# Kernel tuning notes

Hardware: AMD Instinct MI355X
Metric: run time of the kernel (lower is better)

The kernel has to match this reference:

```python
import jax, jax.numpy as jnp
import numpy as np

B, T, C = 2, 2048, 1024
N_HEAD, N_KV_HEAD, N_GLOBAL_HEAD = 16, 8, 8
HEAD_DIM = C // N_HEAD  # 64
Q_PER_KV = N_HEAD // N_KV_HEAD  # 2
N_GLOBAL_KV = N_GLOBAL_HEAD // Q_PER_KV  # 4
VE_GATE_CH = 32


def setup_inputs() -> dict:
    key = jax.random.key(0)
    ks = jax.random.split(key, 8)
    x = jax.random.normal(ks[0], (B, T, C), jnp.float32)
    ve = jax.random.normal(ks[1], (B, T, N_KV_HEAD * HEAD_DIM), jnp.float32)
    # rotary cos/sin: [T, 1, head_dim//2]
    half = HEAD_DIM // 2
    inv_freq = 1.0 / (10000.0 ** (np.arange(half, dtype=np.float32) / half))
    ang = np.arange(T, dtype=np.float32)[:, None] * inv_freq[None, :]
    cos = jnp.asarray(np.cos(ang))[:, None, :]
    sin = jnp.asarray(np.sin(ang))[:, None, :]
    s = 0.02
    Wq = jax.random.normal(ks[2], (C, N_HEAD * HEAD_DIM), jnp.float32) * s
    Wk = jax.random.normal(ks[3], (C, N_KV_HEAD * HEAD_DIM), jnp.float32) * s
    Wv = jax.random.normal(ks[4], (C, N_KV_HEAD * HEAD_DIM), jnp.float32) * s
    Wproj = jax.random.normal(ks[5], (C, C), jnp.float32) * s
    Wgate = jax.random.normal(ks[6], (VE_GATE_CH, N_KV_HEAD), jnp.float32) * s
    return {"x": x, "ve": ve, "cos": cos, "sin": sin, "Wq": Wq, "Wk": Wk,
            "Wv": Wv, "Wproj": Wproj, "Wgate": Wgate, "window": 512}


def _rope(x, cos, sin):
    # x: [B,T,H,D]; cos/sin: [T,1,D/2]
    d = x.shape[-1] // 2
    x1, x2 = x[..., :d], x[..., d:]
    return jnp.concatenate([x1 * cos + x2 * sin, -x1 * sin + x2 * cos], axis=-1)


def _rmsnorm(x):
    eps = jnp.finfo(x.dtype).eps
    return x * jax.lax.rsqrt(jnp.mean(x * x, axis=-1, keepdims=True) + eps)


def _attn(q, k, v, mask):
    # q,k,v: [B,T,H,D]; mask: [T,T] bool (True = allowed)
    scale = 1.0 / jnp.sqrt(jnp.asarray(q.shape[-1], q.dtype))
    scores = jnp.einsum('bqhd,bkhd->bhqk', q, k) * scale
    scores = jnp.where(mask[None, None], scores, jnp.finfo(scores.dtype).min)
    p = jax.nn.softmax(scores, axis=-1)
    return jnp.einsum('bhqk,bkhd->bqhd', p, v)


def reference(x, ve, cos, sin, Wq, Wk, Wv, Wproj, Wgate, window):
    q = (x @ Wq).reshape(B, T, N_HEAD, HEAD_DIM)
    k = (x @ Wk).reshape(B, T, N_KV_HEAD, HEAD_DIM)
    v = (x @ Wv).reshape(B, T, N_KV_HEAD, HEAD_DIM)
    # value-embedding gate
    gate = 2.0 * jax.nn.sigmoid(x[..., :VE_GATE_CH] @ Wgate)  # [B,T,n_kv]
    v = v + gate[..., None] * ve.reshape(B, T, N_KV_HEAD, HEAD_DIM)
    q, k = _rope(q, cos, sin), _rope(k, cos, sin)
    q, k = _rmsnorm(q), _rmsnorm(k)
    # split global / local heads
    qg, ql = q[:, :, :N_GLOBAL_HEAD], q[:, :, N_GLOBAL_HEAD:]
    kg, kl = k[:, :, :N_GLOBAL_KV], k[:, :, N_GLOBAL_KV:]
    vg, vl = v[:, :, :N_GLOBAL_KV], v[:, :, N_GLOBAL_KV:]
    # GQA: expand kv heads
    kg, vg = jnp.repeat(kg, Q_PER_KV, axis=2), jnp.repeat(vg, Q_PER_KV, axis=2)
    kl, vl = jnp.repeat(kl, Q_PER_KV, axis=2), jnp.repeat(vl, Q_PER_KV, axis=2)
    i = jnp.arange(T)[:, None]
    j = jnp.arange(T)[None, :]
    causal = j <= i
    local_mask = causal & (j >= i - window)  # flash window_size=(window, 0)
    yg = _attn(qg, kg, vg, causal)
    yl = _attn(ql, kl, vl, local_mask)
    y = jnp.concatenate([yg, yl], axis=2).reshape(B, T, C)
    return y @ Wproj
```

## Files before the change

kernel.cpp:

```cpp
#include <hip/hip_runtime.h>
#include <hip/hip_bf16.h>

#define BB 2
#define TT 2048
#define CC 1024
#define NH 16
#define NKV 8
#define HD 64

typedef __attribute__((ext_vector_type(8))) short short8;
typedef __attribute__((ext_vector_type(4))) float float4v;
typedef __attribute__((ext_vector_type(4))) unsigned int uint4v;

__device__ __forceinline__ ushort f2bf(float f) {
    __hip_bfloat16 h = __float2bfloat16(f);
    union { __hip_bfloat16 h; ushort u; } v; v.h = h; return v.u;
}
__device__ __forceinline__ float bf2f(ushort u) {
    union { unsigned int i; float f; } v; v.i = ((unsigned int)u) << 16; return v.f;
}

__device__ __forceinline__ float fexp2(float x) {
#if __has_builtin(__builtin_amdgcn_exp2f)
    return __builtin_amdgcn_exp2f(x);
#else
    return __expf(x * 0.69314718056f);
#endif
}

__device__ __forceinline__ void gload16(const ushort* g, ushort* l) {
    __builtin_amdgcn_global_load_lds(
        (const __attribute__((address_space(1))) unsigned int*)g,
        (__attribute__((address_space(3))) unsigned int*)l, 16, 0, 0);
}

__device__ __forceinline__ void transpose_tile(
    const float* __restrict__ src, ushort* __restrict__ dst,
    int Kd, int Nd, int kt, int nt, float* tile )
{
    const int tid = threadIdx.x;
    {
        int r = tid >> 2, c = (tid & 3) * 16;
        #pragma unroll
        for (int i = 0; i < 4; i++) {
            float4 v = *(const float4*)&src[(size_t)(kt + r) * Nd + nt + c + i * 4];
            tile[r * 65 + c + i * 4 + 0] = v.x;
            tile[r * 65 + c + i * 4 + 1] = v.y;
            tile[r * 65 + c + i * 4 + 2] = v.z;
            tile[r * 65 + c + i * 4 + 3] = v.w;
        }
    }
    __syncthreads();
    {
        int n = tid >> 2, k = (tid & 3) * 16;
        #pragma unroll
        for (int i = 0; i < 2; i++) {
            ushort u[8];
            #pragma unroll
            for (int j = 0; j < 8; j++) u[j] = f2bf(tile[(k + i * 8 + j) * 65 + n]);
            *(uint4*)&dst[(size_t)(nt + n) * Kd + kt + k + i * 8] = *(uint4*)u;
        }
    }
}

__global__ __launch_bounds__(256) void prep_kernel(
    const float* __restrict__ x, ushort* __restrict__ xb,
    const float* __restrict__ Wq, const float* __restrict__ Wk,
    const float* __restrict__ Wv, const float* __restrict__ Wproj,
    const float* __restrict__ wgate,
    ushort* __restrict__ WqkvT, ushort* __restrict__ WpT,
    float* __restrict__ gateP)
{
    __shared__ float tile[64 * 65];
    const int bid = blockIdx.x;
    if (bid < 4096) {
        int i = (bid * 256 + threadIdx.x) * 4;
        float4 v = *(const float4*)&x[i];
        xb[i + 0] = f2bf(v.x);
        xb[i + 1] = f2bf(v.y);
        xb[i + 2] = f2bf(v.z);
        xb[i + 3] = f2bf(v.w);
        {
            int g = threadIdx.x >> 5, ii = threadIdx.x & 31;
            float p = x[(size_t)bid * CC + ii] * wgate[ii * 8 + g];
            #pragma unroll
            for (int off = 16; off; off >>= 1) p += __shfl_down(p, off, 32);
            if (ii == 0) gateP[bid * 8 + g] = 2.f / (1.f + __expf(-p));
        }
        return;
    }
    int t = bid - 4096;
    if (t < 256) {
        transpose_tile(Wq, WqkvT, 1024, 1024, (t >> 4) * 64, (t & 15) * 64, tile);
    } else if (t < 384) {
        t -= 256;
        transpose_tile(Wk, WqkvT + (size_t)1024 * 1024, 1024, 512, (t >> 3) * 64, (t & 7) * 64, tile);
    } else if (t < 512) {
        t -= 384;
        transpose_tile(Wv, WqkvT + (size_t)1536 * 1024, 1024, 512, (t >> 3) * 64, (t & 7) * 64, tile);
    } else {
        t -= 512;
        transpose_tile(Wproj, WpT, 1024, 1024, (t >> 4) * 64, (t & 15) * 64, tile);
    }
}

template<int BM, int OBF16>
__global__ __launch_bounds__(256) void gemm_bt_kernel(
    const ushort* __restrict__ A, const ushort* __restrict__ Bt,
    void* __restrict__ Cp, int M, int N, int K, int ldc)
{
    constexpr int RT = BM / 32;
    __shared__ ushort As[BM][32];
    __shared__ ushort Bs[128][32];

    const int m0 = blockIdx.x * BM;
    const int n0 = blockIdx.y * 128;
    const int tid = threadIdx.x;
    const int lane = tid & 63;
    const int w = tid >> 6;
    const int lr = lane & 15, lc = lane >> 4;
    const int wm = (w >> 1) * (BM / 2), wn = (w & 1) * 64;

    float4v acc[RT][4] = {};

    for (int k0 = 0; k0 < K; k0 += 32) {
        #pragma unroll
        for (int s = 0; s < BM / 64; s++) {
            int rb = w * (BM / 4) + s * 16;
            gload16(&A[(size_t)(m0 + rb + (lane >> 2)) * K + k0 + (lane & 3) * 8], &As[rb][0]);
        }
        #pragma unroll
        for (int s = 0; s < 2; s++) {
            int rb = w * 32 + s * 16;
            gload16(&Bt[(size_t)(n0 + rb + (lane >> 2)) * K + k0 + (lane & 3) * 8], &Bs[rb][0]);
        }
        __syncthreads();

        short8 af[RT], bf[4];
        #pragma unroll
        for (int t = 0; t < RT; t++)
            af[t] = *(const short8*)&As[wm + t * 16 + lr][lc * 8];
        #pragma unroll
        for (int t = 0; t < 4; t++)
            bf[t] = *(const short8*)&Bs[wn + t * 16 + lr][lc * 8];
        #pragma unroll
        for (int rt = 0; rt < RT; rt++)
            #pragma unroll
            for (int ct = 0; ct < 4; ct++)
                acc[rt][ct] = __builtin_amdgcn_mfma_f32_16x16x32_bf16(af[rt], bf[ct], acc[rt][ct], 0, 0, 0);
        __syncthreads();
    }

    #pragma unroll
    for (int rt = 0; rt < RT; rt++)
        #pragma unroll
        for (int ct = 0; ct < 4; ct++)
            #pragma unroll
            for (int r = 0; r < 4; r++) {
                int row = m0 + wm + rt * 16 + lc * 4 + r;
                int col = n0 + wn + ct * 16 + lr;
                if (OBF16) ((ushort*)Cp)[(size_t)row * ldc + col] = f2bf(acc[rt][ct][r]);
                else       ((float*)Cp)[(size_t)row * ldc + col] = acc[rt][ct][r];
            }
}

__global__ __launch_bounds__(256) void gemm_qkv_kernel(
    const ushort* __restrict__ A, const ushort* __restrict__ Bt,
    const float* __restrict__ cosb, const float* __restrict__ sinb,
    const float* __restrict__ gateP, const float* __restrict__ ve,
    ushort* __restrict__ Qb, ushort* __restrict__ Kb, ushort* __restrict__ Vn)
{
    constexpr int K = 1024;
    __shared__ ushort As[128][32];
    __shared__ ushort Bs[128][32];

    const int m0 = blockIdx.x * 128;
    const int n0 = blockIdx.y * 128;
    const int tid = threadIdx.x;
    const int lane = tid & 63;
    const int w = tid >> 6;
    const int lr = lane & 15, lc = lane >> 4;
    const int wm = (w >> 1) * 64, wn = (w & 1) * 64;

    float4v acc[4][4] = {};

    for (int k0 = 0; k0 < K; k0 += 32) {
        #pragma unroll
        for (int s = 0; s < 2; s++) {
            int rb = w * 32 + s * 16;
            gload16(&A[(size_t)(m0 + rb + (lane >> 2)) * K + k0 + (lane & 3) * 8], &As[rb][0]);
            gload16(&Bt[(size_t)(n0 + rb + (lane >> 2)) * K + k0 + (lane & 3) * 8], &Bs[rb][0]);
        }
        __syncthreads();

        short8 af[4], bf[4];
        #pragma unroll
        for (int t = 0; t < 4; t++)
            af[t] = *(const short8*)&As[wm + t * 16 + lr][lc * 8];
        #pragma unroll
        for (int t = 0; t < 4; t++)
            bf[t] = *(const short8*)&Bs[wn + t * 16 + lr][lc * 8];
        #pragma unroll
        for (int rt = 0; rt < 4; rt++)
            #pragma unroll
            for (int ct = 0; ct < 4; ct++)
                acc[rt][ct] = __builtin_amdgcn_mfma_f32_16x16x32_bf16(af[rt], bf[ct], acc[rt][ct], 0, 0, 0);
        __syncthreads();
    }

    const int cg = n0 + wn;
    const int hh2 = cg >> 6;

    if (hh2 < 24) {
        #pragma unroll
        for (int rt = 0; rt < 4; rt++) {
            #pragma unroll
            for (int r = 0; r < 4; r++) {
                int row = m0 + wm + rt * 16 + lc * 4 + r;
                int b = row >> 11, t = row & 2047;
                float v0 = acc[rt][0][r], v1 = acc[rt][1][r];
                float v2 = acc[rt][2][r], v3 = acc[rt][3][r];
                const float* cp = &cosb[t * 32];
                const float* sp = &sinb[t * 32];
                float c0 = cp[lr], s0 = sp[lr];
                float c1 = cp[16 + lr], s1 = sp[16 + lr];
                float r0 = v0 * c0 + v2 * s0;
                float r1 = v1 * c1 + v3 * s1;
                float r2 = v2 * c0 - v0 * s0;
                float r3 = v3 * c1 - v1 * s1;
                float ss = (r0 * r0 + r1 * r1) + (r2 * r2 + r3 * r3);
                ss += __shfl_xor(ss, 1);
                ss += __shfl_xor(ss, 2);
                ss += __shfl_xor(ss, 4);
                ss += __shfl_xor(ss, 8);
                float sc = rsqrtf(ss * (1.f / 64.f) + 1.1920929e-07f);
                ushort* op = (hh2 < 16)
                    ? &Qb[(((size_t)b * NH + hh2) * TT + t) * HD]
                    : &Kb[(((size_t)b * NKV + (hh2 - 16)) * TT + t) * HD];
                op[lr]      = f2bf(r0 * sc);
                op[16 + lr] = f2bf(r1 * sc);
                op[32 + lr] = f2bf(r2 * sc);
                op[48 + lr] = f2bf(r3 * sc);
            }
        }
    } else {
        const int kvh = hh2 - 24;
        #pragma unroll
        for (int rt = 0; rt < 4; rt++) {
            #pragma unroll
            for (int r = 0; r < 4; r++) {
                int row = m0 + wm + rt * 16 + lc * 4 + r;
                int b = row >> 11, t = row & 2047;
                float g = gateP[row * 8 + kvh];
                const float* vp = &ve[(size_t)row * 512 + kvh * 64];
                ushort* op = &Vn[(((size_t)b * NKV + kvh) * TT + t) * HD];
                op[lr]      = f2bf(acc[rt][0][r] + g * vp[lr]);
                op[16 + lr] = f2bf(acc[rt][1][r] + g * vp[16 + lr]);
                op[32 + lr] = f2bf(acc[rt][2][r] + g * vp[32 + lr]);
                op[48 + lr] = f2bf(acc[rt][3][r] + g * vp[48 + lr]);
            }
        }
    }
}

__global__ __launch_bounds__(256) void v_transpose_kernel(
    const ushort* __restrict__ Vn, ushort* __restrict__ Vt)
{
    __shared__ ushort tile[64][72];
    const int t0 = blockIdx.x * 64;
    const int bh = blockIdx.y;
    const ushort* src = &Vn[(size_t)bh * TT * HD + (size_t)t0 * HD];
    ushort* dst = &Vt[(size_t)bh * HD * TT + t0];
    const int tid = threadIdx.x;
    {
        int r = tid >> 2, c = (tid & 3) * 16;
        #pragma unroll
        for (int i = 0; i < 2; i++)
            *(uint4*)&tile[r][c + i * 8] = *(const uint4*)&src[(size_t)r * HD + c + i * 8];
    }
    __syncthreads();
    {
        int d = tid >> 2, c = (tid & 3) * 16;
        #pragma unroll
        for (int i = 0; i < 2; i++) {
            ushort u[8];
            #pragma unroll
            for (int j = 0; j < 8; j++) u[j] = tile[c + i * 8 + j][d];
            *(uint4*)&dst[(size_t)d * TT + c + i * 8] = *(uint4*)u;
        }
    }
}

__global__ __launch_bounds__(256) void attn_kernel(
    const ushort* __restrict__ Qb, const ushort* __restrict__ Kb,
    const ushort* __restrict__ Vt, ushort* __restrict__ Yb,
    const int* __restrict__ winp)
{
    const int gid = blockIdx.x;
    int b, h, qw;
    if (gid < 1024) { qw = 63 - (gid >> 4); h = (gid >> 1) & 7; b = gid & 1; }
    else { int j = gid - 1024; qw = 63 - (j >> 4); h = 8 + ((j >> 1) & 7); b = j & 1; }

    const int q0 = qw * 32;
    const int kvh = h >> 1;
    const bool local = (h >= 8);
    int window = *winp;
    if (window < 0 || window > TT) window = TT;
    const int tid = threadIdx.x;
    const int w = tid >> 6;
    const int lane = tid & 63;
    const int lr = lane & 15, lc = lane >> 4;

    __shared__ float4v Ol[4][4][64];
    __shared__ float Ll[4][16];

    const ushort* qbase = &Qb[(((size_t)b * NH + h) * TT + q0) * HD];
    short8 qf[2][2];
    #pragma unroll
    for (int rt = 0; rt < 2; rt++)
        #pragma unroll
        for (int xh = 0; xh < 2; xh++)
            qf[rt][xh] = *(const short8*)&qbase[(size_t)(rt * 16 + lr) * HD + xh * 32 + lc * 8];

    float4v o[2][4] = {};
    float l_[2] = {0.f, 0.f};

    const ushort* Kbase = &Kb[((size_t)b * NKV + kvh) * TT * HD];
    const ushort* Vbase = &Vt[((size_t)b * NKV + kvh) * HD * TT];

    const int qlast = q0 + 31;
    int jstart = 0;
    if (local) { int js = q0 - window; if (js > 0) jstart = js & ~63; }
    const int j0first = jstart + w * 64;

    const float ESC = 0.1803368801f;

    short8 kf[4][2];
    if (j0first <= qlast) {
        #pragma unroll
        for (int jt = 0; jt < 4; jt++) {
            const ushort* kp = &Kbase[(size_t)(j0first + jt * 16 + lr) * HD + lc * 8];
            kf[jt][0] = *(const short8*)kp;
            kf[jt][1] = *(const short8*)(kp + 32);
        }
    }

    for (int j0 = j0first; j0 <= qlast; j0 += 256) {
        short8 vf[4][2];
        #pragma unroll
        for (int ct = 0; ct < 4; ct++) {
            const ushort* vp = &Vbase[(size_t)(ct * 16 + lr) * TT + j0 + lc * 8];
            vf[ct][0] = *(const short8*)vp;
            vf[ct][1] = *(const short8*)(vp + 32);
        }
        short8 kn[4][2];
        const bool more = (j0 + 256 <= qlast);
        if (more) {
            #pragma unroll
            for (int jt = 0; jt < 4; jt++) {
                const ushort* kp = &Kbase[(size_t)(j0 + 256 + jt * 16 + lr) * HD + lc * 8];
                kn[jt][0] = *(const short8*)kp;
                kn[jt][1] = *(const short8*)(kp + 32);
            }
        }

        float4v st[2][4];
        #pragma unroll
        for (int jt = 0; jt < 4; jt++)
            #pragma unroll
            for (int rt = 0; rt < 2; rt++) {
                float4v z = {};
                z = __builtin_amdgcn_mfma_f32_16x16x32_bf16(kf[jt][0], qf[rt][0], z, 0, 0, 0);
                z = __builtin_amdgcn_mfma_f32_16x16x32_bf16(kf[jt][1], qf[rt][1], z, 0, 0, 0);
                st[rt][jt] = z;
            }

        const bool need_c = (j0 + 63 > q0);
        const bool need_w = local && (j0 < qlast - window);

        #pragma unroll
        for (int rt = 0; rt < 2; rt++) {
            const int qrow = q0 + rt * 16 + lr;
            float p[4][4];
            if (need_c || need_w) {
                #pragma unroll
                for (int jt = 0; jt < 4; jt++)
                    #pragma unroll
                    for (int r = 0; r < 4; r++) {
                        int key = j0 + jt * 16 + lc * 4 + r;
                        bool ok = (key <= qrow) && (!local || key >= qrow - window);
                        p[jt][r] = ok ? fexp2(st[rt][jt][r] * ESC) : 0.f;
                    }
            } else {
                #pragma unroll
                for (int jt = 0; jt < 4; jt++)
                    #pragma unroll
                    for (int r = 0; r < 4; r++)
                        p[jt][r] = fexp2(st[rt][jt][r] * ESC);
            }
            float s0 = (p[0][0] + p[0][1]) + (p[0][2] + p[0][3]);
            float s1 = (p[1][0] + p[1][1]) + (p[1][2] + p[1][3]);
            float s2 = (p[2][0] + p[2][1]) + (p[2][2] + p[2][3]);
            float s3 = (p[3][0] + p[3][1]) + (p[3][2] + p[3][3]);
            l_[rt] += (s0 + s1) + (s2 + s3);

            unsigned int a0, a1, b0, b1, c0, c1, d0, d1;
            asm("v_cvt_pk_bf16_f32 %0, %1, %2" : "=v"(a0) : "v"(p[0][0]), "v"(p[0][1]));
            asm("v_cvt_pk_bf16_f32 %0, %1, %2" : "=v"(a1) : "v"(p[0][2]), "v"(p[0][3]));
            asm("v_cvt_pk_bf16_f32 %0, %1, %2" : "=v"(b0) : "v"(p[1][0]), "v"(p[1][1]));
            asm("v_cvt_pk_bf16_f32 %0, %1, %2" : "=v"(b1) : "v"(p[1][2]), "v"(p[1][3]));
            asm("v_cvt_pk_bf16_f32 %0, %1, %2" : "=v"(c0) : "v"(p[2][0]), "v"(p[2][1]));
            asm("v_cvt_pk_bf16_f32 %0, %1, %2" : "=v"(c1) : "v"(p[2][2]), "v"(p[2][3]));
            asm("v_cvt_pk_bf16_f32 %0, %1, %2" : "=v"(d0) : "v"(p[3][0]), "v"(p[3][1]));
            asm("v_cvt_pk_bf16_f32 %0, %1, %2" : "=v"(d1) : "v"(p[3][2]), "v"(p[3][3]));

            asm("v_permlane32_swap_b32 %0, %1" : "+v"(a0), "+v"(b0));
            asm("v_permlane16_swap_b32 %0, %1" : "+v"(a0), "+v"(b0));
            asm("v_permlane32_swap_b32 %0, %1" : "+v"(a1), "+v"(b1));
            asm("v_permlane16_swap_b32 %0, %1" : "+v"(a1), "+v"(b1));
            asm("v_permlane32_swap_b32 %0, %1" : "+v"(c0), "+v"(d0));
            asm("v_permlane16_swap_b32 %0, %1" : "+v"(c0), "+v"(d0));
            asm("v_permlane32_swap_b32 %0, %1" : "+v"(c1), "+v"(d1));
            asm("v_permlane16_swap_b32 %0, %1" : "+v"(c1), "+v"(d1));

            uint4v u0 = {a0, a1, b0, b1};
            uint4v u1 = {c0, c1, d0, d1};
            short8 P0 = __builtin_bit_cast(short8, u0);
            short8 P1 = __builtin_bit_cast(short8, u1);

            #pragma unroll
            for (int ct = 0; ct < 4; ct++) {
                o[rt][ct] = __builtin_amdgcn_mfma_f32_16x16x32_bf16(vf[ct][0], P0, o[rt][ct], 0, 0, 0);
                o[rt][ct] = __builtin_amdgcn_mfma_f32_16x16x32_bf16(vf[ct][1], P1, o[rt][ct], 0, 0, 0);
            }
        }

        if (more) {
            #pragma unroll
            for (int jt = 0; jt < 4; jt++) {
                kf[jt][0] = kn[jt][0];
                kf[jt][1] = kn[jt][1];
            }
        }
    }

    #pragma unroll
    for (int rt = 0; rt < 2; rt++) {
        l_[rt] += __shfl_xor(l_[rt], 16);
        l_[rt] += __shfl_xor(l_[rt], 32);
    }

    #pragma unroll
    for (int rt = 0; rt < 2; rt++) {
        #pragma unroll
        for (int ct = 0; ct < 4; ct++) Ol[w][ct][lane] = o[rt][ct];
        if (lc == 0) Ll[w][lr] = l_[rt];
        __syncthreads();

        {
            const int ct = w;
            float ltot = (Ll[0][lr] + Ll[1][lr]) + (Ll[2][lr] + Ll[3][lr]);
            float inv = 1.f / fmaxf(ltot, 1e-20f);
            float4v a0 = Ol[0][ct][lane], a1 = Ol[1][ct][lane];
            float4v a2 = Ol[2][ct][lane], a3 = Ol[3][ct][lane];
            int qrow = q0 + rt * 16 + lr;
            ushort4 u;
            u.x = f2bf(((a0[0] + a1[0]) + (a2[0] + a3[0])) * inv);
            u.y = f2bf(((a0[1] + a1[1]) + (a2[1] + a3[1])) * inv);
            u.z = f2bf(((a0[2] + a1[2]) + (a2[2] + a3[2])) * inv);
            u.w = f2bf(((a0[3] + a1[3]) + (a2[3] + a3[3])) * inv);
            *(ushort4*)&Yb[((size_t)b * TT + qrow) * CC + h * 64 + ct * 16 + lc * 4] = u;
        }
        if (rt == 0) __syncthreads();
    }
}

extern "C" void kernel_launch(void* const* d_in, const int* in_sizes, int n_in,
                              void* d_out, int out_size, void* d_ws, size_t ws_size,
                              hipStream_t stream) {
    (void)in_sizes; (void)n_in; (void)out_size; (void)ws_size;
    const float* x     = (const float*)d_in[0];
    const float* ve    = (const float*)d_in[1];
    const float* cosb  = (const float*)d_in[2];
    const float* sinb  = (const float*)d_in[3];
    const float* Wq    = (const float*)d_in[4];
    const float* Wk    = (const float*)d_in[5];
    const float* Wv    = (const float*)d_in[6];
    const float* Wproj = (const float*)d_in[7];
    const float* Wgate = (const float*)d_in[8];
    const int*   winp  = (const int*)d_in[9];
    float* out = (float*)d_out;

    char* ws = (char*)d_ws;
    ushort* Yb    = (ushort*)ws;
    float*  gateP = (float*)(ws + 8388608);
    ushort* Vnb   = (ushort*)(ws + 12582912);
    ushort* xb    = (ushort*)(ws + 33554432);
    ushort* WqkvT = (ushort*)(ws + 41943040);
    ushort* WpT   = (ushort*)(ws + 46137344);
    ushort* Qb    = (ushort*)(ws + 48234496);
    ushort* Kb    = (ushort*)(ws + 56623104);
    ushort* Vtb   = (ushort*)(ws + 60817408);

    dim3 blk(256);
    prep_kernel<<<dim3(4864), blk, 0, stream>>>(x, xb, Wq, Wk, Wv, Wproj, Wgate, WqkvT, WpT, gateP);
    gemm_qkv_kernel<<<dim3(32, 16), blk, 0, stream>>>(xb, WqkvT, cosb, sinb, gateP, ve, Qb, Kb, Vnb);
    v_transpose_kernel<<<dim3(TT / 64, BB * NKV), blk, 0, stream>>>(Vnb, Vtb);
    attn_kernel<<<dim3(2048), blk, 0, stream>>>(Qb, Kb, Vtb, Yb, winp);
    gemm_bt_kernel<64, 0><<<dim3(64, 8), blk, 0, stream>>>(Yb, WpT, out, 4096, 1024, 1024, 1024);
}
```

Before: 203.1 us.

## Double-buffer LDS tiles in GEMM kernels to overlap global loads with MFMA

```diff
diff --git a/kernel.cpp b/kernel.cpp
--- a/kernel.cpp
+++ b/kernel.cpp
@@ -32,6 +32,10 @@
     __builtin_amdgcn_global_load_lds(
         (const __attribute__((address_space(1))) unsigned int*)g,
         (__attribute__((address_space(3))) unsigned int*)l, 16, 0, 0);
+}
+
+__device__ __forceinline__ void vmcnt0() {
+    asm volatile("s_waitcnt vmcnt(0)" ::: "memory");
 }
 
 __device__ __forceinline__ void transpose_tile(
@@ -110,8 +114,8 @@
     void* __restrict__ Cp, int M, int N, int K, int ldc)
 {
     constexpr int RT = BM / 32;
-    __shared__ ushort As[BM][32];
-    __shared__ ushort Bs[128][32];
+    __shared__ ushort As[2][BM][32];
+    __shared__ ushort Bs[2][128][32];
 
     const int m0 = blockIdx.x * BM;
     const int n0 = blockIdx.y * 128;
@@ -121,33 +125,53 @@
     const int lr = lane & 15, lc = lane >> 4;
     const int wm = (w >> 1) * (BM / 2), wn = (w & 1) * 64;
 
+    const int arow = lane >> 2, acol = (lane & 3) * 8;
+
     float4v acc[RT][4] = {};
 
+    #pragma unroll
+    for (int s = 0; s < BM / 64; s++) {
+        int rb = w * (BM / 4) + s * 16;
+        gload16(&A[(size_t)(m0 + rb + arow) * K + acol], &As[0][rb][0]);
+    }
+    #pragma unroll
+    for (int s = 0; s < 2; s++) {
+        int rb = w * 32 + s * 16;
+        gload16(&Bt[(size_t)(n0 + rb + arow) * K + acol], &Bs[0][rb][0]);
+    }
+    vmcnt0();
+    __syncthreads();
+
     for (int k0 = 0; k0 < K; k0 += 32) {
-        #pragma unroll
-        for (int s = 0; s < BM / 64; s++) {
-            int rb = w * (BM / 4) + s * 16;
-            gload16(&A[(size_t)(m0 + rb + (lane >> 2)) * K + k0 + (lane & 3) * 8], &As[rb][0]);
-        }
-        #pragma unroll
-        for (int s = 0; s < 2; s++) {
-            int rb = w * 32 + s * 16;
-            gload16(&Bt[(size_t)(n0 + rb + (lane >> 2)) * K + k0 + (lane & 3) * 8], &Bs[rb][0]);
-        }
-        __syncthreads();
+        const int cur = (k0 >> 5) & 1;
+        if (k0 + 32 < K) {
+            const int kn = k0 + 32;
+            #pragma unroll
+            for (int s = 0; s < BM / 64; s++) {
+                int rb = w * (BM / 4) + s * 16;
+                gload16(&A[(size_t)(m0 + rb + arow) * K + kn + acol], &As[cur ^ 1][rb][0]);
+            }
+            #pragma unroll
+            for (int s = 0; s < 2; s++) {
+                int rb = w * 32 + s * 16;
+                gload16(&Bt[(size_t)(n0 + rb + arow) * K + kn + acol], &Bs[cur ^ 1][rb][0]);
+            }
+        }
 
         short8 af[RT], bf[4];
         #pragma unroll
         for (int t = 0; t < RT; t++)
-            af[t] = *(const short8*)&As[wm + t * 16 + lr][lc * 8];
+            af[t] = *(const short8*)&As[cur][wm + t * 16 + lr][lc * 8];
         #pragma unroll
         for (int t = 0; t < 4; t++)
-            bf[t] = *(const short8*)&Bs[wn + t * 16 + lr][lc * 8];
+            bf[t] = *(const short8*)&Bs[cur][wn + t * 16 + lr][lc * 8];
         #pragma unroll
         for (int rt = 0; rt < RT; rt++)
             #pragma unroll
             for (int ct = 0; ct < 4; ct++)
                 acc[rt][ct] = __builtin_amdgcn_mfma_f32_16x16x32_bf16(af[rt], bf[ct], acc[rt][ct], 0, 0, 0);
+
+        vmcnt0();
         __syncthreads();
     }
 
@@ -171,8 +195,8 @@
     ushort* __restrict__ Qb, ushort* __restrict__ Kb, ushort* __restrict__ Vn)
 {
     constexpr int K = 1024;
-    __shared__ ushort As[128][32];
-    __shared__ ushort Bs[128][32];
+    __shared__ ushort As[2][128][32];
+    __shared__ ushort Bs[2][128][32];
 
     const int m0 = blockIdx.x * 128;
     const int n0 = blockIdx.y * 128;
@@ -182,29 +206,45 @@
     const int lr = lane & 15, lc = lane >> 4;
     const int wm = (w >> 1) * 64, wn = (w & 1) * 64;
 
+    const int arow = lane >> 2, acol = (lane & 3) * 8;
+
     float4v acc[4][4] = {};
 
+    #pragma unroll
+    for (int s = 0; s < 2; s++) {
+        int rb = w * 32 + s * 16;
+        gload16(&A[(size_t)(m0 + rb + arow) * K + acol], &As[0][rb][0]);
+        gload16(&Bt[(size_t)(n0 + rb + arow) * K + acol], &Bs[0][rb][0]);
+    }
+    vmcnt0();
+    __syncthreads();
+
     for (int k0 = 0; k0 < K; k0 += 32) {
-        #pragma unroll
-        for (int s = 0; s < 2; s++) {
-            int rb = w * 32 + s * 16;
-            gload16(&A[(size_t)(m0 + rb + (lane >> 2)) * K + k0 + (lane & 3) * 8], &As[rb][0]);
-            gload16(&Bt[(size_t)(n0 + rb + (lane >> 2)) * K + k0 + (lane & 3) * 8], &Bs[rb][0]);
-        }
-        __syncthreads();
+        const int cur = (k0 >> 5) & 1;
+        if (k0 + 32 < K) {
+            const int kn = k0 + 32;
+            #pragma unroll
+            for (int s = 0; s < 2; s++) {
+                int rb = w * 32 + s * 16;
+                gload16(&A[(size_t)(m0 + rb + arow) * K + kn + acol], &As[cur ^ 1][rb][0]);
+                gload16(&Bt[(size_t)(n0 + rb + arow) * K + kn + acol], &Bs[cur ^ 1][rb][0]);
+            }
+        }
 
         short8 af[4], bf[4];
         #pragma unroll
         for (int t = 0; t < 4; t++)
-            af[t] = *(const short8*)&As[wm + t * 16 + lr][lc * 8];
+            af[t] = *(const short8*)&As[cur][wm + t * 16 + lr][lc * 8];
         #pragma unroll
         for (int t = 0; t < 4; t++)
-            bf[t] = *(const short8*)&Bs[wn + t * 16 + lr][lc * 8];
+            bf[t] = *(const short8*)&Bs[cur][wn + t * 16 + lr][lc * 8];
         #pragma unroll
         for (int rt = 0; rt < 4; rt++)
             #pragma unroll
             for (int ct = 0; ct < 4; ct++)
                 acc[rt][ct] = __builtin_amdgcn_mfma_f32_16x16x32_bf16(af[rt], bf[ct], acc[rt][ct], 0, 0, 0);
+
+        vmcnt0();
         __syncthreads();
     }
 
```

Result: slower. 207.4 us (+2.1%).
